# Performance work log

Measured on AMD Instinct MI355X. Metric: run time of the kernel, lower is better.

The kernel has to match this reference:

```python
import jax, jax.numpy as jnp
import numpy as np

N_NODES = 100_000
N_EDGES = 800_000
D_IN = 64
HID = 32   # hidden_channels
OUT = 64   # out_channels
H1, H2, H3 = 7, 4, 1


def _lin(key, din, dout, scale=0.05):
    k1, k2 = jax.random.split(key)
    W = jax.random.normal(k1, (din, dout), jnp.float32) * scale
    b = jax.random.normal(k2, (dout,), jnp.float32) * scale
    return W, b


def setup_inputs() -> dict:
    key = jax.random.key(0)
    ks = jax.random.split(key, 16)
    x = jax.random.normal(ks[0], (N_NODES, D_IN), jnp.float32)
    edge_index = jax.random.randint(ks[1], (2, N_EDGES), 0, N_NODES, dtype=jnp.int32)
    inp = {"x": x, "edge_index": edge_index}
    # (in_dim, heads, per-head channels) for the 3 TransformerConv layers
    dims = [(D_IN, H1, HID), (H1 * HID, H2, HID), (H2 * HID, H3, OUT)]
    i = 2
    for l, (din, h, c) in enumerate(dims, start=1):
        for nm in ("q", "k", "v", "s"):  # query, key, value, skip linears
            W, b = _lin(ks[i], din, h * c)
            i += 1
            inp[f"W{nm}{l}"] = W
            inp[f"b{nm}{l}"] = b
    return inp


def _transformer_conv(x, src, dst, Wq, bq, Wk, bk, Wv, bv, Ws, bs, H, C):
    # PyG TransformerConv (concat=True, beta=False, root_weight=True, no edge feats)
    q = (x @ Wq + bq).reshape(-1, H, C)
    k = (x @ Wk + bk).reshape(-1, H, C)
    v = (x @ Wv + bv).reshape(-1, H, C)
    # per-edge attention logits [E, H]
    alpha = jnp.einsum('ehc,ehc->eh', q[dst], k[src]) / jnp.sqrt(jnp.asarray(C, q.dtype))
    # segment softmax over incoming edges of each dst node
    amax = jax.ops.segment_max(alpha, dst, num_segments=N_NODES)
    ex = jnp.exp(alpha - amax[dst])
    denom = jax.ops.segment_sum(ex, dst, num_segments=N_NODES)
    attn = ex / (denom[dst] + 1e-16)
    # weighted message aggregation [N, H, C] -> [N, H*C]
    msg = v[src] * attn[..., None]
    out = jax.ops.segment_sum(msg, dst, num_segments=N_NODES).reshape(N_NODES, H * C)
    # root/skip connection
    return out + x @ Ws + bs


def reference(x, edge_index,
              Wq1, bq1, Wk1, bk1, Wv1, bv1, Ws1, bs1,
              Wq2, bq2, Wk2, bk2, Wv2, bv2, Ws2, bs2,
              Wq3, bq3, Wk3, bk3, Wv3, bv3, Ws3, bs3):
    src, dst = edge_index[0], edge_index[1]
    h = jax.nn.relu(_transformer_conv(x, src, dst, Wq1, bq1, Wk1, bk1, Wv1, bv1, Ws1, bs1, H1, HID))
    h = jax.nn.relu(_transformer_conv(h, src, dst, Wq2, bq2, Wk2, bk2, Wv2, bv2, Ws2, bs2, H2, HID))
    return _transformer_conv(h, src, dst, Wq3, bq3, Wk3, bk3, Wv3, bv3, Ws3, bs3, H3, OUT)
```

## Files before the change

kernel.cpp:

```cpp
#include <hip/hip_runtime.h>
#include <hip/hip_bf16.h>
#include <hip/hip_fp8.h>
#include <math.h>

#define N_NODES 100000
#define N_EDGES 800000
#define SCAN_BLOCKS 98

typedef __attribute__((ext_vector_type(8))) short short8;
typedef __attribute__((ext_vector_type(4))) float f32x4;
typedef __attribute__((ext_vector_type(2))) float f32x2;

__device__ __forceinline__ unsigned short f2b(float f) {
    __hip_bfloat16 h = __float2bfloat16(f);
    return *reinterpret_cast<unsigned short*>(&h);
}
__device__ __forceinline__ float2 up2(unsigned u) {
    unsigned lo = u << 16;
    unsigned hi = u & 0xffff0000u;
    float2 r;
    __builtin_memcpy(&r.x, &lo, 4);
    __builtin_memcpy(&r.y, &hi, 4);
    return r;
}
__device__ __forceinline__ unsigned char f2fp8(float f) {
#if __has_builtin(__builtin_amdgcn_cvt_pk_fp8_f32)
    unsigned u = __builtin_amdgcn_cvt_pk_fp8_f32(f, f, 0u, false);
    return (unsigned char)(u & 0xffu);
#else
    __hip_fp8_e4m3 h(f);
    return (unsigned char)h.__x;
#endif
}
__device__ __forceinline__ float dotk(float2 qa, float2 qb, unsigned k4) {
#if __has_builtin(__builtin_amdgcn_cvt_pk_f32_fp8)
    f32x2 lo = __builtin_amdgcn_cvt_pk_f32_fp8(k4, false);
    f32x2 hi = __builtin_amdgcn_cvt_pk_f32_fp8(k4, true);
    float p = lo[0] * qa.x;
    p = fmaf(lo[1], qa.y, p);
    p = fmaf(hi[0], qb.x, p);
    p = fmaf(hi[1], qb.y, p);
    return p;
#else
    __hip_fp8_e4m3 a, b, c, d;
    a.__x = (unsigned char)k4;
    b.__x = (unsigned char)(k4 >> 8);
    c.__x = (unsigned char)(k4 >> 16);
    d.__x = (unsigned char)(k4 >> 24);
    float p = (float)a * qa.x;
    p = fmaf((float)b, qa.y, p);
    p = fmaf((float)c, qb.x, p);
    p = fmaf((float)d, qb.y, p);
    return p;
#endif
}
__device__ __forceinline__ float dot4(float2 qa, float2 qb, unsigned k0, unsigned k1) {
    float2 x = up2(k0), y = up2(k1);
    float p = x.x * qa.x;
    p = fmaf(x.y, qa.y, p);
    p = fmaf(y.x, qb.x, p);
    p = fmaf(y.y, qb.y, p);
    return p;
}


__global__ void hist_kernel(const int* __restrict__ dst, int* __restrict__ deg) {
    int e = blockIdx.x * blockDim.x + threadIdx.x;
    if (e < N_EDGES) atomicAdd(&deg[dst[e]], 1);
}

__global__ __launch_bounds__(1024) void scan_part(const int* __restrict__ deg,
                                                  int* __restrict__ rowptr,
                                                  int* __restrict__ partials) {
    __shared__ int buf[1024];
    const int t = threadIdx.x;
    const int i = blockIdx.x * 1024 + t;
    int x = (i < N_NODES) ? deg[i] : 0;
    buf[t] = x;
    __syncthreads();
    for (int off = 1; off < 1024; off <<= 1) {
        int y = (t >= off) ? buf[t - off] : 0;
        __syncthreads();
        buf[t] += y;
        __syncthreads();
    }
    if (i < N_NODES) rowptr[i] = buf[t] - x;
    if (t == 1023) partials[blockIdx.x] = buf[t];
}

__global__ __launch_bounds__(128) void scan_tail(int* __restrict__ partials,
                                                 int* __restrict__ rowptr) {
    __shared__ int buf[128];
    const int t = threadIdx.x;
    int x = (t < SCAN_BLOCKS) ? partials[t] : 0;
    buf[t] = x;
    __syncthreads();
    for (int off = 1; off < 128; off <<= 1) {
        int y = (t >= off) ? buf[t - off] : 0;
        __syncthreads();
        buf[t] += y;
        __syncthreads();
    }
    if (t < SCAN_BLOCKS) partials[t] = buf[t] - x;
    if (t == 127) rowptr[N_NODES] = buf[127];
}

__global__ __launch_bounds__(1024) void scan_add(int* __restrict__ rowptr,
                                                 const int* __restrict__ partials) {
    const int i = blockIdx.x * 1024 + threadIdx.x;
    if (i < N_NODES) rowptr[i] += partials[blockIdx.x];
}

__global__ void scatter_kernel(const int* __restrict__ src, const int* __restrict__ dst,
                               const int* __restrict__ rowptr, int* __restrict__ cursor,
                               int* __restrict__ sorted_src) {
    int e = blockIdx.x * blockDim.x + threadIdx.x;
    if (e < N_EDGES) {
        int d = dst[e];
        int pos = atomicAdd(&cursor[d], 1);
        sorted_src[rowptr[d] + pos] = src[e];
    }
}

__global__ void fill_kernel(float* __restrict__ out, int n, float val) {
    int i = blockIdx.x * blockDim.x + threadIdx.x;
    if (i < n) out[i] = val;
}


__global__ void convert_kernel(const float* __restrict__ X, unsigned short* __restrict__ Y, int n4) {
    int i = blockIdx.x * blockDim.x + threadIdx.x;
    if (i < n4) {
        float4 f = ((const float4*)X)[i];
        ushort4 u;
        u.x = f2b(f.x); u.y = f2b(f.y); u.z = f2b(f.z); u.w = f2b(f.w);
        ((ushort4*)Y)[i] = u;
    }
}

__global__ void build_wt(const float* __restrict__ Wq, const float* __restrict__ Wk,
                         const float* __restrict__ Wv, const float* __restrict__ Wsk,
                         const float* __restrict__ bq, const float* __restrict__ bk,
                         const float* __restrict__ bv, const float* __restrict__ bsk,
                         unsigned short* __restrict__ WT, float* __restrict__ biasF,
                         int K, int HC, int C, int mode) {
    int total = 4 * HC * K;
    int idx = blockIdx.x * blockDim.x + threadIdx.x;
    if (idx >= total) return;
    int rowc = idx / K;
    int kk = idx - rowc * K;
    const float* W;
    const float* Bp;
    int cw;
    if (mode == 0) {
        if (rowc < HC)          { W = Wq;  Bp = bq;  cw = rowc; }
        else if (rowc < 2 * HC) { W = Wv;  Bp = bv;  cw = rowc - HC; }
        else if (rowc < 3 * HC) { W = Wk;  Bp = bk;  cw = rowc - 2 * HC; }
        else                    { W = Wsk; Bp = bsk; cw = rowc - 3 * HC; }
    } else {
        if (rowc < HC) {
            W = Wq; Bp = bq; cw = rowc;
        } else if (rowc < 3 * HC) {
            int u = rowc - HC;
            int h = u / (2 * C);
            int rr = u - h * 2 * C;
            int grp = rr >> 3, w = rr & 7;
            if (w < 4) { W = Wk; Bp = bk; cw = h * C + grp * 4 + w; }
            else       { W = Wv; Bp = bv; cw = h * C + grp * 4 + w - 4; }
        } else {
            W = Wsk; Bp = bsk; cw = rowc - 3 * HC;
        }
    }
    WT[idx] = f2b(W[(size_t)kk * HC + cw]);
    if (kk == 0) biasF[rowc] = Bp[cw];
}


template <int K, int YMODE>
__global__ __launch_bounds__(256) void mfma_gemm(
    const unsigned short* __restrict__ Xb, const unsigned short* __restrict__ WT,
    const float* __restrict__ biasF, void* __restrict__ Y,
    int ncols, int ostride, int split, int rq, int rkv) {
    constexpr int STR = 40;
    constexpr int ESTR = 136;
    __shared__ __align__(16) char smem[128 * ESTR * 2];
    unsigned short* Xs = (unsigned short*)smem;
    unsigned short* Ws = (unsigned short*)(smem + 128 * STR * 2);
    const int t = threadIdx.x;
    const int wave = t >> 6, lane = t & 63, quad = lane >> 4, l16 = lane & 15;
    const int n0 = blockIdx.x * 128, c0 = blockIdx.y * 128;

    f32x4 acc[2][8];
#pragma unroll
    for (int i = 0; i < 2; ++i)
#pragma unroll
        for (int j = 0; j < 8; ++j)
#pragma unroll
            for (int r = 0; r < 4; ++r) acc[i][j][r] = 0.f;

    for (int k0 = 0; k0 < K; k0 += 32) {
#pragma unroll
        for (int i = 0; i < 2; ++i) {
            int idx = t + i * 256;
            int row = idx >> 2;
            int seg = (idx & 3) << 3;
            int gr = n0 + row;
            short8 xv;
#pragma unroll
            for (int z = 0; z < 8; ++z) xv[z] = 0;
            if (gr < N_NODES)
                xv = *(const short8*)(Xb + (size_t)gr * K + k0 + seg);
            *(short8*)(&Xs[row * STR + seg]) = xv;

            int c = c0 + row;
            short8 wv;
#pragma unroll
            for (int z = 0; z < 8; ++z) wv[z] = 0;
            if (c < ncols) {
                int wtrow = (c < split) ? (rq + c) : (rkv + (c - split));
                wv = *(const short8*)(WT + (size_t)wtrow * K + k0 + seg);
            }
            *(short8*)(&Ws[row * STR + seg]) = wv;
        }
        __syncthreads();

        short8 af0 = *(short8*)(&Xs[(wave * 32 + l16) * STR + quad * 8]);
        short8 af1 = *(short8*)(&Xs[(wave * 32 + 16 + l16) * STR + quad * 8]);
#pragma unroll
        for (int ct = 0; ct < 8; ++ct) {
            short8 bfr = *(short8*)(&Ws[(ct * 16 + l16) * STR + quad * 8]);
            acc[0][ct] = __builtin_amdgcn_mfma_f32_16x16x32_bf16(af0, bfr, acc[0][ct], 0, 0, 0);
            acc[1][ct] = __builtin_amdgcn_mfma_f32_16x16x32_bf16(af1, bfr, acc[1][ct], 0, 0, 0);
        }
        __syncthreads();
    }

    if constexpr (YMODE == 1) {
        unsigned short* Es = (unsigned short*)smem;
#pragma unroll
        for (int ct = 0; ct < 8; ++ct) {
            if (c0 + ct * 16 >= ncols) break;
            int col = c0 + ct * 16 + l16;
            int brow = (col < split) ? (rq + col) : (rkv + (col - split));
            float bv = biasF[brow];
#pragma unroll
            for (int rt = 0; rt < 2; ++rt)
#pragma unroll
                for (int r = 0; r < 4; ++r) {
                    int row = wave * 32 + rt * 16 + quad * 4 + r;
                    Es[row * ESTR + ct * 16 + l16] = f2b(acc[rt][ct][r] + bv);
                }
        }
        __syncthreads();
        const int erow = t >> 1;
        const int cb = (t & 1) * 8;
        const int gr = n0 + erow;
#pragma unroll
        for (int j = 0; j < 8; ++j) {
            int gc = c0 + j * 16 + cb;
            if (gr < N_NODES && gc < ncols)
                *(short8*)((unsigned short*)Y + (size_t)gr * ostride + gc) =
                    *(const short8*)(&Es[erow * ESTR + j * 16 + cb]);
        }
    } else if constexpr (YMODE == 2) {
        constexpr int EB = 144;
        unsigned char* Es = (unsigned char*)smem;
#pragma unroll
        for (int ct = 0; ct < 8; ++ct) {
            if (c0 + ct * 16 >= ncols) break;
            int col = c0 + ct * 16 + l16;
            int brow = (col < split) ? (rq + col) : (rkv + (col - split));
            float bv = biasF[brow];
#pragma unroll
            for (int rt = 0; rt < 2; ++rt)
#pragma unroll
                for (int r = 0; r < 4; ++r) {
                    int row = wave * 32 + rt * 16 + quad * 4 + r;
                    Es[row * EB + ct * 16 + l16] = f2fp8(acc[rt][ct][r] + bv);
                }
        }
        __syncthreads();
        const int erow = t >> 1;
        const int q8 = (t & 1) * 64;
        const int gr = n0 + erow;
#pragma unroll
        for (int j = 0; j < 4; ++j) {
            int gc = c0 + q8 + j * 16;
            if (gr < N_NODES && gc < ncols)
                *(uint4*)((unsigned char*)Y + (size_t)gr * ostride + gc) =
                    *(const uint4*)(&Es[erow * EB + q8 + j * 16]);
        }
    } else {
#pragma unroll
        for (int ct = 0; ct < 8; ++ct) {
            int col = c0 + ct * 16 + l16;
            if (col >= ncols) continue;
            int brow = (col < split) ? (rq + col) : (rkv + (col - split));
            float bv = biasF[brow];
#pragma unroll
            for (int rt = 0; rt < 2; ++rt) {
#pragma unroll
                for (int r = 0; r < 4; ++r) {
                    int row = n0 + wave * 32 + rt * 16 + quad * 4 + r;
                    if (row < N_NODES)
                        ((float*)Y)[(size_t)row * ostride + col] = acc[rt][ct][r] + bv;
                }
            }
        }
    }
}

template <int K, int YMODE>
static inline void launch_gemm(const unsigned short* Xb, const unsigned short* WT,
                               const float* biasF, void* Y, int ncols, int ostride,
                               int split, int rq, int rkv, hipStream_t s) {
    const int GX = (N_NODES + 127) / 128;
    int ny = (ncols + 127) / 128;
    mfma_gemm<K, YMODE><<<dim3(GX, ny), 256, 0, s>>>(
        Xb, WT, biasF, Y, ncols, ostride, split, rq, rkv);
}


template <int C, int NH, bool RELU, bool YBF, bool KF8>
__global__ __launch_bounds__(256) void attn3(
    const unsigned short* __restrict__ F, const unsigned char* __restrict__ K8,
    const int* __restrict__ rowptr, const int* __restrict__ ssrc,
    void* __restrict__ Hv, int h0, int ostride) {
    constexpr int LPN = NH * C / 4;
    constexpr int NPW = 64 / LPN;
    constexpr int gC = NH * C;
    constexpr int Ms = KF8 ? (2 * gC) : (3 * gC);
    const int lane = threadIdx.x & 63;
    const int wave = (blockIdx.x * 256 + threadIdx.x) >> 6;
    const int slot = lane / LPN;
    const int cl = lane - slot * LPN;
    const int n = wave * NPW + slot;
    if (slot >= NPW || n >= N_NODES) return;

    const int head = cl / (C / 4);
    const int c4 = (cl - head * (C / 4)) * 4;
    const int qoff = head * C + c4;
    const int voff = gC + qoff;
    const int kvoff = gC + head * 2 * C + 2 * c4;
    const float SCALE2 = ((C == 64) ? 0.125f : 0.17677669529663687f) * 1.44269504f;

    uint2 qu = *(const uint2*)(F + (size_t)n * Ms + qoff);
    float2 qa = up2(qu.x), qb = up2(qu.y);
    qa.x *= SCALE2; qa.y *= SCALE2; qb.x *= SCALE2; qb.y *= SCALE2;
    int s0 = rowptr[n], s1 = rowptr[n + 1];

    float l = 0.f, a0 = 0.f, a1 = 0.f, a2 = 0.f, a3 = 0.f;
    int ei = s0;
    if constexpr (KF8) {
        for (; ei + 3 < s1; ei += 4) {
            int iA = ssrc[ei], iB = ssrc[ei + 1], iC = ssrc[ei + 2], iD = ssrc[ei + 3];
            unsigned kA = *(const unsigned*)(K8 + (size_t)iA * gC + qoff);
            unsigned kB = *(const unsigned*)(K8 + (size_t)iB * gC + qoff);
            unsigned kC = *(const unsigned*)(K8 + (size_t)iC * gC + qoff);
            unsigned kD = *(const unsigned*)(K8 + (size_t)iD * gC + qoff);
            uint2 vAu = *(const uint2*)(F + (size_t)iA * Ms + voff);
            uint2 vBu = *(const uint2*)(F + (size_t)iB * Ms + voff);
            uint2 vCu = *(const uint2*)(F + (size_t)iC * Ms + voff);
            uint2 vDu = *(const uint2*)(F + (size_t)iD * Ms + voff);
            float pA = dotk(qa, qb, kA);
            float pB = dotk(qa, qb, kB);
            float pC = dotk(qa, qb, kC);
            float pD = dotk(qa, qb, kD);
#pragma unroll
            for (int off = C / 8; off > 0; off >>= 1) {
                pA += __shfl_xor(pA, off);
                pB += __shfl_xor(pB, off);
                pC += __shfl_xor(pC, off);
                pD += __shfl_xor(pD, off);
            }
            float eA = exp2f(pA), eB = exp2f(pB), eC = exp2f(pC), eD = exp2f(pD);
            l += (eA + eB) + (eC + eD);
            float2 vA0 = up2(vAu.x), vA1 = up2(vAu.y);
            float2 vB0 = up2(vBu.x), vB1 = up2(vBu.y);
            float2 vC0 = up2(vCu.x), vC1 = up2(vCu.y);
            float2 vD0 = up2(vDu.x), vD1 = up2(vDu.y);
            a0 = fmaf(eA, vA0.x, fmaf(eB, vB0.x, fmaf(eC, vC0.x, fmaf(eD, vD0.x, a0))));
            a1 = fmaf(eA, vA0.y, fmaf(eB, vB0.y, fmaf(eC, vC0.y, fmaf(eD, vD0.y, a1))));
            a2 = fmaf(eA, vA1.x, fmaf(eB, vB1.x, fmaf(eC, vC1.x, fmaf(eD, vD1.x, a2))));
            a3 = fmaf(eA, vA1.y, fmaf(eB, vB1.y, fmaf(eC, vC1.y, fmaf(eD, vD1.y, a3))));
        }
        if (ei + 1 < s1) {
            int iA = ssrc[ei], iB = ssrc[ei + 1];
            ei += 2;
            unsigned kA = *(const unsigned*)(K8 + (size_t)iA * gC + qoff);
            unsigned kB = *(const unsigned*)(K8 + (size_t)iB * gC + qoff);
            uint2 vAu = *(const uint2*)(F + (size_t)iA * Ms + voff);
            uint2 vBu = *(const uint2*)(F + (size_t)iB * Ms + voff);
            float pA = dotk(qa, qb, kA);
            float pB = dotk(qa, qb, kB);
#pragma unroll
            for (int off = C / 8; off > 0; off >>= 1) {
                pA += __shfl_xor(pA, off);
                pB += __shfl_xor(pB, off);
            }
            float eA = exp2f(pA), eB = exp2f(pB);
            l += eA + eB;
            float2 vA0 = up2(vAu.x), vA1 = up2(vAu.y);
            float2 vB0 = up2(vBu.x), vB1 = up2(vBu.y);
            a0 = fmaf(eA, vA0.x, fmaf(eB, vB0.x, a0));
            a1 = fmaf(eA, vA0.y, fmaf(eB, vB0.y, a1));
            a2 = fmaf(eA, vA1.x, fmaf(eB, vB1.x, a2));
            a3 = fmaf(eA, vA1.y, fmaf(eB, vB1.y, a3));
        }
        if (ei < s1) {
            int iA = ssrc[ei];
            unsigned kA = *(const unsigned*)(K8 + (size_t)iA * gC + qoff);
            uint2 vAu = *(const uint2*)(F + (size_t)iA * Ms + voff);
            float pA = dotk(qa, qb, kA);
#pragma unroll
            for (int off = C / 8; off > 0; off >>= 1) pA += __shfl_xor(pA, off);
            float eA = exp2f(pA);
            l += eA;
            float2 vA0 = up2(vAu.x), vA1 = up2(vAu.y);
            a0 = fmaf(eA, vA0.x, a0);
            a1 = fmaf(eA, vA0.y, a1);
            a2 = fmaf(eA, vA1.x, a2);
            a3 = fmaf(eA, vA1.y, a3);
        }
    } else {
        for (; ei + 3 < s1; ei += 4) {
            int iA = ssrc[ei], iB = ssrc[ei + 1], iC = ssrc[ei + 2], iD = ssrc[ei + 3];
            uint4 A = *(const uint4*)(F + (size_t)iA * Ms + kvoff);
            uint4 B = *(const uint4*)(F + (size_t)iB * Ms + kvoff);
            uint4 Cv = *(const uint4*)(F + (size_t)iC * Ms + kvoff);
            uint4 D = *(const uint4*)(F + (size_t)iD * Ms + kvoff);
            float pA = dot4(qa, qb, A.x, A.y);
            float pB = dot4(qa, qb, B.x, B.y);
            float pC = dot4(qa, qb, Cv.x, Cv.y);
            float pD = dot4(qa, qb, D.x, D.y);
#pragma unroll
            for (int off = C / 8; off > 0; off >>= 1) {
                pA += __shfl_xor(pA, off);
                pB += __shfl_xor(pB, off);
                pC += __shfl_xor(pC, off);
                pD += __shfl_xor(pD, off);
            }
            float eA = exp2f(pA), eB = exp2f(pB), eC = exp2f(pC), eD = exp2f(pD);
            l += (eA + eB) + (eC + eD);
            float2 vA0 = up2(A.z), vA1 = up2(A.w);
            float2 vB0 = up2(B.z), vB1 = up2(B.w);
            float2 vC0 = up2(Cv.z), vC1 = up2(Cv.w);
            float2 vD0 = up2(D.z), vD1 = up2(D.w);
            a0 = fmaf(eA, vA0.x, fmaf(eB, vB0.x, fmaf(eC, vC0.x, fmaf(eD, vD0.x, a0))));
            a1 = fmaf(eA, vA0.y, fmaf(eB, vB0.y, fmaf(eC, vC0.y, fmaf(eD, vD0.y, a1))));
            a2 = fmaf(eA, vA1.x, fmaf(eB, vB1.x, fmaf(eC, vC1.x, fmaf(eD, vD1.x, a2))));
            a3 = fmaf(eA, vA1.y, fmaf(eB, vB1.y, fmaf(eC, vC1.y, fmaf(eD, vD1.y, a3))));
        }
        if (ei + 1 < s1) {
            int iA = ssrc[ei], iB = ssrc[ei + 1];
            ei += 2;
            uint4 A = *(const uint4*)(F + (size_t)iA * Ms + kvoff);
            uint4 B = *(const uint4*)(F + (size_t)iB * Ms + kvoff);
            float pA = dot4(qa, qb, A.x, A.y);
            float pB = dot4(qa, qb, B.x, B.y);
#pragma unroll
            for (int off = C / 8; off > 0; off >>= 1) {
                pA += __shfl_xor(pA, off);
                pB += __shfl_xor(pB, off);
            }
            float eA = exp2f(pA), eB = exp2f(pB);
            l += eA + eB;
            float2 vA0 = up2(A.z), vA1 = up2(A.w);
            float2 vB0 = up2(B.z), vB1 = up2(B.w);
            a0 = fmaf(eA, vA0.x, fmaf(eB, vB0.x, a0));
            a1 = fmaf(eA, vA0.y, fmaf(eB, vB0.y, a1));
            a2 = fmaf(eA, vA1.x, fmaf(eB, vB1.x, a2));
            a3 = fmaf(eA, vA1.y, fmaf(eB, vB1.y, a3));
        }
        if (ei < s1) {
            int iA = ssrc[ei];
            uint4 A = *(const uint4*)(F + (size_t)iA * Ms + kvoff);
            float pA = dot4(qa, qb, A.x, A.y);
#pragma unroll
            for (int off = C / 8; off > 0; off >>= 1) pA += __shfl_xor(pA, off);
            float eA = exp2f(pA);
            l += eA;
            float2 vA0 = up2(A.z), vA1 = up2(A.w);
            a0 = fmaf(eA, vA0.x, a0);
            a1 = fmaf(eA, vA0.y, a1);
            a2 = fmaf(eA, vA1.x, a2);
            a3 = fmaf(eA, vA1.y, a3);
        }
    }

    float inv = 1.f / (l + 1e-16f);
    float r0 = a0 * inv, r1 = a1 * inv, r2 = a2 * inv, r3 = a3 * inv;

    const int col = (h0 + head) * C + c4;
    if constexpr (YBF) {
        uint2* Hp = (uint2*)((unsigned short*)Hv + (size_t)n * ostride + col);
        uint2 hv = *Hp;
        float2 hx = up2(hv.x), hy = up2(hv.y);
        float o0 = hx.x + r0, o1 = hx.y + r1, o2 = hy.x + r2, o3 = hy.y + r3;
        if (RELU) {
            o0 = fmaxf(o0, 0.f); o1 = fmaxf(o1, 0.f);
            o2 = fmaxf(o2, 0.f); o3 = fmaxf(o3, 0.f);
        }
        uint2 pv;
        pv.x = (unsigned)f2b(o0) | ((unsigned)f2b(o1) << 16);
        pv.y = (unsigned)f2b(o2) | ((unsigned)f2b(o3) << 16);
        *Hp = pv;
    } else {
        float4* Hp = (float4*)((float*)Hv + (size_t)n * ostride + col);
        float4 h = *Hp;
        h.x += r0; h.y += r1; h.z += r2; h.w += r3;
        if (RELU) {
            h.x = fmaxf(h.x, 0.f); h.y = fmaxf(h.y, 0.f);
            h.z = fmaxf(h.z, 0.f); h.w = fmaxf(h.w, 0.f);
        }
        *Hp = h;
    }
}

static inline void launch_attn32(int NH, int h0, const unsigned short* F,
                                 const unsigned char* K8, void* H, int ostride,
                                 const int* rowptr, const int* ssrc, hipStream_t stream) {
    switch (NH) {
        case 1: attn3<32, 1, true, true, true><<<3125, 256, 0, stream>>>(F, K8, rowptr, ssrc, H, h0, ostride); break;
        case 2: attn3<32, 2, true, true, true><<<6250, 256, 0, stream>>>(F, K8, rowptr, ssrc, H, h0, ostride); break;
        case 3: attn3<32, 3, true, true, true><<<12500, 256, 0, stream>>>(F, K8, rowptr, ssrc, H, h0, ostride); break;
        case 4: attn3<32, 4, true, true, true><<<12500, 256, 0, stream>>>(F, K8, rowptr, ssrc, H, h0, ostride); break;
        default: attn3<32, 7, true, true, true><<<25000, 256, 0, stream>>>(F, K8, rowptr, ssrc, H, h0, ostride); break;
    }
}


extern "C" void kernel_launch(void* const* d_in, const int* in_sizes, int n_in,
                              void* d_out, int out_size, void* d_ws, size_t ws_size,
                              hipStream_t stream) {
    const float* x = (const float*)d_in[0];
    const int* ei = (const int*)d_in[1];
    const int* srcp = ei;
    const int* dstp = ei + N_EDGES;

    const float* W[12];
    const float* B[12];
    for (int i = 0; i < 12; ++i) {
        W[i] = (const float*)d_in[2 + 2 * i];
        B[i] = (const float*)d_in[3 + 2 * i];
    }
    float* out = (float*)d_out;

    char* p = (char*)d_ws;
    size_t off = 0;
    unsigned short* wt  = (unsigned short*)(p + off); off += 240000;
    float* biasF        = (float*)(p + off);          off += 4096;
    int* rowptr = (int*)(p + off); off += sizeof(int) * (N_NODES + 1);
    int* deg    = (int*)(p + off); off += sizeof(int) * N_NODES;
    int* cursor = (int*)(p + off); off += sizeof(int) * N_NODES;
    int* partials = (int*)(p + off); off += sizeof(int) * 128;
    int* ssrc   = (int*)(p + off); off += sizeof(int) * N_EDGES;
    off = (off + 255) & ~(size_t)255;
    unsigned short* h1  = (unsigned short*)(p + off); off += (size_t)224 * N_NODES * 2;
    unsigned short* h2  = (unsigned short*)(p + off); off += (size_t)128 * N_NODES * 2;
    unsigned short* xb1 = (unsigned short*)(p + off); off += (size_t)64 * N_NODES * 2;
    unsigned short* tail = (unsigned short*)(p + off);

    if (ws_size < off + 6500000) {
        fill_kernel<<<(out_size + 255) / 256, 256, 0, stream>>>(out, out_size, (float)(ws_size >> 20));
        return;
    }
    size_t tail_bytes = ws_size - off;
    const size_t F1PASS = (size_t)3 * 32 * N_NODES * 2;

    int nh1[7], np1 = 0;
    int nh2[4], np2 = 0;
    unsigned short *F1w, *F2w;
    if (tail_bytes >= 7 * F1PASS) {
        nh1[np1++] = 7;
        nh2[np2++] = 4;
        F1w = F2w = tail;
    } else if (tail_bytes >= 4 * F1PASS) {
        nh1[np1++] = 4; nh1[np1++] = 3;
        nh2[np2++] = 4;
        F1w = F2w = tail;
    } else if (tail_bytes >= 2 * F1PASS) {
        nh1[np1++] = 2; nh1[np1++] = 2; nh1[np1++] = 2; nh1[np1++] = 1;
        nh2[np2++] = 2; nh2[np2++] = 2;
        F1w = F2w = tail;
    } else {
        for (int i = 0; i < 7; ++i) nh1[np1++] = 1;
        for (int i = 0; i < 4; ++i) nh2[np2++] = 1;
        F1w = h2;
        F2w = xb1;
    }
    unsigned short* F3 = h1;

    hipMemsetAsync(deg, 0, sizeof(int) * 2 * N_NODES, stream);
    hist_kernel<<<(N_EDGES + 255) / 256, 256, 0, stream>>>(dstp, deg);
    scan_part<<<SCAN_BLOCKS, 1024, 0, stream>>>(deg, rowptr, partials);
    scan_tail<<<1, 128, 0, stream>>>(partials, rowptr);
    scan_add<<<SCAN_BLOCKS, 1024, 0, stream>>>(rowptr, partials);
    scatter_kernel<<<(N_EDGES + 255) / 256, 256, 0, stream>>>(srcp, dstp, rowptr, cursor, ssrc);

    convert_kernel<<<(N_NODES * 64 / 4 + 255) / 256, 256, 0, stream>>>(x, xb1, N_NODES * 64 / 4);

    build_wt<<<(4 * 224 * 64 + 255) / 256, 256, 0, stream>>>(
        W[0], W[1], W[2], W[3], B[0], B[1], B[2], B[3], wt, biasF, 64, 224, 32, 0);
    launch_gemm<64, 1>(xb1, wt + (size_t)3 * 224 * 64, biasF + 3 * 224, h1,
                       224, 224, 224, 0, 0, stream);
    {
        int h0 = 0;
        for (int pass = 0; pass < np1; ++pass) {
            int NH = nh1[pass];
            int nc = NH * 32;
            unsigned char* K1w = (unsigned char*)F1w + (size_t)4 * nc * N_NODES;
            launch_gemm<64, 1>(xb1, wt, biasF, F1w, 2 * nc, 2 * nc,
                               nc, h0 * 32, 224 + h0 * 32, stream);
            launch_gemm<64, 2>(xb1, wt, biasF, K1w, nc, nc,
                               nc, 2 * 224 + h0 * 32, 0, stream);
            launch_attn32(NH, h0, F1w, K1w, h1, 224, rowptr, ssrc, stream);
            h0 += NH;
        }
    }

    build_wt<<<(4 * 128 * 224 + 255) / 256, 256, 0, stream>>>(
        W[4], W[5], W[6], W[7], B[4], B[5], B[6], B[7], wt, biasF, 224, 128, 32, 0);
    launch_gemm<224, 1>(h1, wt + (size_t)3 * 128 * 224, biasF + 3 * 128, h2,
                        128, 128, 128, 0, 0, stream);
    {
        int h0 = 0;
        for (int pass = 0; pass < np2; ++pass) {
            int NH = nh2[pass];
            int nc = NH * 32;
            unsigned char* K2w = (unsigned char*)F2w + (size_t)4 * nc * N_NODES;
            launch_gemm<224, 1>(h1, wt, biasF, F2w, 2 * nc, 2 * nc,
                                nc, h0 * 32, 128 + h0 * 32, stream);
            launch_gemm<224, 2>(h1, wt, biasF, K2w, nc, nc,
                                nc, 2 * 128 + h0 * 32, 0, stream);
            launch_attn32(NH, h0, F2w, K2w, h2, 128, rowptr, ssrc, stream);
            h0 += NH;
        }
    }

    build_wt<<<(4 * 64 * 128 + 255) / 256, 256, 0, stream>>>(
        W[8], W[9], W[10], W[11], B[8], B[9], B[10], B[11], wt, biasF, 128, 64, 64, 1);
    launch_gemm<128, 1>(h2, wt, biasF, F3, 192, 192,
                        64, 0, 64, stream);
    launch_gemm<128, 0>(h2, wt + (size_t)3 * 64 * 128, biasF + 3 * 64, out,
                        64, 64, 64, 0, 0, stream);
    attn3<64, 1, false, false, false><<<6250, 256, 0, stream>>>(F3, (const unsigned char*)nullptr,
                                                                rowptr, ssrc, out, 0, 64);
}
```

Before: 664.9 us.

## Store layer-1 values in FP8 interleaved with keys for single gather

Layer 1 now stores V in FP8 alongside K, interleaved per head and channel group, so each edge needs one 8-byte gather for both K and V instead of a 4-byte FP8 K load plus an 8-byte bf16 V load. The GEMM epilogue writes K and V together into an interleaved FP8 buffer, and the Q buffer shrinks to bf16 Q only. The aim is to cut gather traffic in the edge-bound attention loop. The trade-off is extra quantization error on V from FP8 e4m3.

```diff
diff --git a/kernel.cpp b/kernel.cpp
--- a/kernel.cpp
+++ b/kernel.cpp
@@ -53,6 +53,22 @@
     p = fmaf((float)d, qb.y, p);
     return p;
 #endif
+}
+__device__ __forceinline__ f32x4 up4f8(unsigned v) {
+    f32x4 r;
+#if __has_builtin(__builtin_amdgcn_cvt_pk_f32_fp8)
+    f32x2 lo = __builtin_amdgcn_cvt_pk_f32_fp8(v, false);
+    f32x2 hi = __builtin_amdgcn_cvt_pk_f32_fp8(v, true);
+    r[0] = lo[0]; r[1] = lo[1]; r[2] = hi[0]; r[3] = hi[1];
+#else
+    __hip_fp8_e4m3 a, b, c, d;
+    a.__x = (unsigned char)v;
+    b.__x = (unsigned char)(v >> 8);
+    c.__x = (unsigned char)(v >> 16);
+    d.__x = (unsigned char)(v >> 24);
+    r[0] = (float)a; r[1] = (float)b; r[2] = (float)c; r[3] = (float)d;
+#endif
+    return r;
 }
 __device__ __forceinline__ float dot4(float2 qa, float2 qb, unsigned k0, unsigned k1) {
     float2 x = up2(k0), y = up2(k1);
@@ -321,7 +337,7 @@
 }
 
 
-template <int C, int NH, bool RELU, bool YBF, bool KF8>
+template <int C, int NH, bool RELU, bool YBF, int KVM>
 __global__ __launch_bounds__(256) void attn3(
     const unsigned short* __restrict__ F, const unsigned char* __restrict__ K8,
     const int* __restrict__ rowptr, const int* __restrict__ ssrc,
@@ -329,7 +345,8 @@
     constexpr int LPN = NH * C / 4;
     constexpr int NPW = 64 / LPN;
     constexpr int gC = NH * C;
-    constexpr int Ms = KF8 ? (2 * gC) : (3 * gC);
+    constexpr int Ms = (KVM == 1) ? gC : (KVM == 2) ? (2 * gC) : (3 * gC);
+    constexpr int Mk = 2 * gC;
     const int lane = threadIdx.x & 63;
     const int wave = (blockIdx.x * 256 + threadIdx.x) >> 6;
     const int slot = lane / LPN;
@@ -341,6 +358,7 @@
     const int c4 = (cl - head * (C / 4)) * 4;
     const int qoff = head * C + c4;
     const int voff = gC + qoff;
+    const int kv8off = 2 * (head * C + c4);
     const int kvoff = gC + head * 2 * C + 2 * c4;
     const float SCALE2 = ((C == 64) ? 0.125f : 0.17677669529663687f) * 1.44269504f;
 
@@ -351,7 +369,67 @@
 
     float l = 0.f, a0 = 0.f, a1 = 0.f, a2 = 0.f, a3 = 0.f;
     int ei = s0;
-    if constexpr (KF8) {
+    if constexpr (KVM == 1) {
+        for (; ei + 3 < s1; ei += 4) {
+            int iA = ssrc[ei], iB = ssrc[ei + 1], iC = ssrc[ei + 2], iD = ssrc[ei + 3];
+            uint2 A = *(const uint2*)(K8 + (size_t)iA * Mk + kv8off);
+            uint2 B = *(const uint2*)(K8 + (size_t)iB * Mk + kv8off);
+            uint2 Cu = *(const uint2*)(K8 + (size_t)iC * Mk + kv8off);
+            uint2 D = *(const uint2*)(K8 + (size_t)iD * Mk + kv8off);
+            float pA = dotk(qa, qb, A.x);
+            float pB = dotk(qa, qb, B.x);
+            float pC = dotk(qa, qb, Cu.x);
+            float pD = dotk(qa, qb, D.x);
+#pragma unroll
+            for (int off = C / 8; off > 0; off >>= 1) {
+                pA += __shfl_xor(pA, off);
+                pB += __shfl_xor(pB, off);
+                pC += __shfl_xor(pC, off);
+                pD += __shfl_xor(pD, off);
+            }
+            float eA = exp2f(pA), eB = exp2f(pB), eC = exp2f(pC), eD = exp2f(pD);
+            l += (eA + eB) + (eC + eD);
+            f32x4 vA = up4f8(A.y), vB = up4f8(B.y), vC = up4f8(Cu.y), vD = up4f8(D.y);
+            a0 = fmaf(eA, vA[0], fmaf(eB, vB[0], fmaf(eC, vC[0], fmaf(eD, vD[0], a0))));
+            a1 = fmaf(eA, vA[1], fmaf(eB, vB[1], fmaf(eC, vC[1], fmaf(eD, vD[1], a1))));
+            a2 = fmaf(eA, vA[2], fmaf(eB, vB[2], fmaf(eC, vC[2], fmaf(eD, vD[2], a2))));
+            a3 = fmaf(eA, vA[3], fmaf(eB, vB[3], fmaf(eC, vC[3], fmaf(eD, vD[3], a3))));
+        }
+        if (ei + 1 < s1) {
+            int iA = ssrc[ei], iB = ssrc[ei + 1];
+            ei += 2;
+            uint2 A = *(const uint2*)(K8 + (size_t)iA * Mk + kv8off);
+            uint2 B = *(const uint2*)(K8 + (size_t)iB * Mk + kv8off);
+            float pA = dotk(qa, qb, A.x);
+            float pB = dotk(qa, qb, B.x);
+#pragma unroll
+            for (int off = C / 8; off > 0; off >>= 1) {
+                pA += __shfl_xor(pA, off);
+                pB += __shfl_xor(pB, off);
+            }
+            float eA = exp2f(pA), eB = exp2f(pB);
+            l += eA + eB;
+            f32x4 vA = up4f8(A.y), vB = up4f8(B.y);
+            a0 = fmaf(eA, vA[0], fmaf(eB, vB[0], a0));
+            a1 = fmaf(eA, vA[1], fmaf(eB, vB[1], a1));
+            a2 = fmaf(eA, vA[2], fmaf(eB, vB[2], a2));
+            a3 = fmaf(eA, vA[3], fmaf(eB, vB[3], a3));
+        }
+        if (ei < s1) {
+            int iA = ssrc[ei];
+            uint2 A = *(const uint2*)(K8 + (size_t)iA * Mk + kv8off);
+            float pA = dotk(qa, qb, A.x);
+#pragma unroll
+            for (int off = C / 8; off > 0; off >>= 1) pA += __shfl_xor(pA, off);
+            float eA = exp2f(pA);
+            l += eA;
+            f32x4 vA = up4f8(A.y);
+            a0 = fmaf(eA, vA[0], a0);
+            a1 = fmaf(eA, vA[1], a1);
+            a2 = fmaf(eA, vA[2], a2);
+            a3 = fmaf(eA, vA[3], a3);
+        }
+    } else if constexpr (KVM == 2) {
         for (; ei + 3 < s1; ei += 4) {
             int iA = ssrc[ei], iB = ssrc[ei + 1], iC = ssrc[ei + 2], iD = ssrc[ei + 3];
             unsigned kA = *(const unsigned*)(K8 + (size_t)iA * gC + qoff);
@@ -517,15 +595,26 @@
     }
 }
 
-static inline void launch_attn32(int NH, int h0, const unsigned short* F,
-                                 const unsigned char* K8, void* H, int ostride,
-                                 const int* rowptr, const int* ssrc, hipStream_t stream) {
+static inline void launch_attn_L1(int NH, int h0, const unsigned short* F,
+                                  const unsigned char* KV8, void* H, int ostride,
+                                  const int* rowptr, const int* ssrc, hipStream_t stream) {
     switch (NH) {
-        case 1: attn3<32, 1, true, true, true><<<3125, 256, 0, stream>>>(F, K8, rowptr, ssrc, H, h0, ostride); break;
-        case 2: attn3<32, 2, true, true, true><<<6250, 256, 0, stream>>>(F, K8, rowptr, ssrc, H, h0, ostride); break;
-        case 3: attn3<32, 3, true, true, true><<<12500, 256, 0, stream>>>(F, K8, rowptr, ssrc, H, h0, ostride); break;
-        case 4: attn3<32, 4, true, true, true><<<12500, 256, 0, stream>>>(F, K8, rowptr, ssrc, H, h0, ostride); break;
-        default: attn3<32, 7, true, true, true><<<25000, 256, 0, stream>>>(F, K8, rowptr, ssrc, H, h0, ostride); break;
+        case 1: attn3<32, 1, true, true, 1><<<3125, 256, 0, stream>>>(F, KV8, rowptr, ssrc, H, h0, ostride); break;
+        case 2: attn3<32, 2, true, true, 1><<<6250, 256, 0, stream>>>(F, KV8, rowptr, ssrc, H, h0, ostride); break;
+        case 3: attn3<32, 3, true, true, 1><<<12500, 256, 0, stream>>>(F, KV8, rowptr, ssrc, H, h0, ostride); break;
+        case 4: attn3<32, 4, true, true, 1><<<12500, 256, 0, stream>>>(F, KV8, rowptr, ssrc, H, h0, ostride); break;
+        default: attn3<32, 7, true, true, 1><<<25000, 256, 0, stream>>>(F, KV8, rowptr, ssrc, H, h0, ostride); break;
+    }
+}
+
+static inline void launch_attn_L2(int NH, int h0, const unsigned short* F,
+                                  const unsigned char* K8, void* H, int ostride,
+                                  const int* rowptr, const int* ssrc, hipStream_t stream) {
+    switch (NH) {
+        case 1: attn3<32, 1, true, true, 2><<<3125, 256, 0, stream>>>(F, K8, rowptr, ssrc, H, h0, ostride); break;
+        case 2: attn3<32, 2, true, true, 2><<<6250, 256, 0, stream>>>(F, K8, rowptr, ssrc, H, h0, ostride); break;
+        case 3: attn3<32, 3, true, true, 2><<<12500, 256, 0, stream>>>(F, K8, rowptr, ssrc, H, h0, ostride); break;
+        default: attn3<32, 4, true, true, 2><<<12500, 256, 0, stream>>>(F, K8, rowptr, ssrc, H, h0, ostride); break;
     }
 }
 
@@ -601,7 +690,7 @@
     convert_kernel<<<(N_NODES * 64 / 4 + 255) / 256, 256, 0, stream>>>(x, xb1, N_NODES * 64 / 4);
 
     build_wt<<<(4 * 224 * 64 + 255) / 256, 256, 0, stream>>>(
-        W[0], W[1], W[2], W[3], B[0], B[1], B[2], B[3], wt, biasF, 64, 224, 32, 0);
+        W[0], W[1], W[2], W[3], B[0], B[1], B[2], B[3], wt, biasF, 64, 224, 32, 1);
     launch_gemm<64, 1>(xb1, wt + (size_t)3 * 224 * 64, biasF + 3 * 224, h1,
                        224, 224, 224, 0, 0, stream);
     {
@@ -609,12 +698,12 @@
         for (int pass = 0; pass < np1; ++pass) {
             int NH = nh1[pass];
             int nc = NH * 32;
-            unsigned char* K1w = (unsigned char*)F1w + (size_t)4 * nc * N_NODES;
-            launch_gemm<64, 1>(xb1, wt, biasF, F1w, 2 * nc, 2 * nc,
-                               nc, h0 * 32, 224 + h0 * 32, stream);
-            launch_gemm<64, 2>(xb1, wt, biasF, K1w, nc, nc,
-                               nc, 2 * 224 + h0 * 32, 0, stream);
-            launch_attn32(NH, h0, F1w, K1w, h1, 224, rowptr, ssrc, stream);
+            unsigned char* K1w = (unsigned char*)F1w + (size_t)2 * nc * N_NODES;
+            launch_gemm<64, 1>(xb1, wt, biasF, F1w, nc, nc,
+                               nc, h0 * 32, 0, stream);
+            launch_gemm<64, 2>(xb1, wt, biasF, K1w, 2 * nc, 2 * nc,
+                               2 * nc, 224 + 2 * h0 * 32, 0, stream);
+            launch_attn_L1(NH, h0, F1w, K1w, h1, 224, rowptr, ssrc, stream);
             h0 += NH;
         }
     }
@@ -633,7 +722,7 @@
                                 nc, h0 * 32, 128 + h0 * 32, stream);
             launch_gemm<224, 2>(h1, wt, biasF, K2w, nc, nc,
                                 nc, 2 * 128 + h0 * 32, 0, stream);
-            launch_attn32(NH, h0, F2w, K2w, h2, 128, rowptr, ssrc, stream);
+            launch_attn_L2(NH, h0, F2w, K2w, h2, 128, rowptr, ssrc, stream);
             h0 += NH;
         }
     }
@@ -644,6 +733,6 @@
                         64, 0, 64, stream);
     launch_gemm<128, 0>(h2, wt + (size_t)3 * 64 * 128, biasF + 3 * 64, out,
                         64, 64, 64, 0, 0, stream);
-    attn3<64, 1, false, false, false><<<6250, 256, 0, stream>>>(F3, (const unsigned char*)nullptr,
-                                                                rowptr, ssrc, out, 0, 64);
-}
+    attn3<64, 1, false, false, 0><<<6250, 256, 0, stream>>>(F3, (const unsigned char*)nullptr,
+                                                            rowptr, ssrc, out, 0, 64);
+}
```

Result: faster. 633.4 us (-4.7%).
